# Kernel optimization log

Hardware: AMD Instinct MI355X
Metric: run time of the kernel (lower is better)

## Reference

```python
import jax, jax.numpy as jnp
import numpy as np

HEADS = 4
HID = 32
IN = 128
OUT = 8
N = 50000
E = 1600000


def setup_inputs() -> dict:
    key = jax.random.key(0)
    ks = jax.random.split(key, 12)
    x = jax.random.normal(ks[0], (N, IN), dtype=jnp.float32)
    edge_index = jax.random.randint(ks[1], (2, E), 0, N, dtype=jnp.int64)
    s = 0.05
    W1 = jax.random.normal(ks[2], (IN, HEADS * HID), dtype=jnp.float32) * s
    att_src1 = jax.random.normal(ks[3], (HEADS, HID), dtype=jnp.float32) * s
    att_dst1 = jax.random.normal(ks[4], (HEADS, HID), dtype=jnp.float32) * s
    b1 = jnp.zeros((HEADS * HID,), dtype=jnp.float32)
    W2 = jax.random.normal(ks[5], (HEADS * HID, HEADS * HID), dtype=jnp.float32) * s
    att_src2 = jax.random.normal(ks[6], (HEADS, HID), dtype=jnp.float32) * s
    att_dst2 = jax.random.normal(ks[7], (HEADS, HID), dtype=jnp.float32) * s
    b2 = jnp.zeros((HEADS * HID,), dtype=jnp.float32)
    Wout = jax.random.normal(ks[8], (HEADS * HID, OUT), dtype=jnp.float32) * s
    bout = jnp.zeros((OUT,), dtype=jnp.float32)
    return {"x": x, "edge_index": edge_index, "W1": W1, "att_src1": att_src1,
            "att_dst1": att_dst1, "b1": b1, "W2": W2, "att_src2": att_src2,
            "att_dst2": att_dst2, "b2": b2, "Wout": Wout, "bout": bout}


def gat_conv(x, src, dst, W, att_src, att_dst, b):
    n = x.shape[0]
    h = (x @ W).reshape(n, HEADS, HID)              # [N,H,C]
    a_s = (h * att_src).sum(-1)                      # [N,H]
    a_d = (h * att_dst).sum(-1)                      # [N,H]
    e = jax.nn.leaky_relu(a_s[src] + a_d[dst], 0.2)  # [E,H]
    # scatter-softmax over incoming edges of each destination node
    m = jax.ops.segment_max(e, dst, num_segments=n)
    e = jnp.exp(e - m[dst])
    denom = jax.ops.segment_sum(e, dst, num_segments=n)
    alpha = e / (denom[dst] + 1e-16)                 # [E,H]
    msg = h[src] * alpha[:, :, None]                 # [E,H,C]
    out = jax.ops.segment_sum(msg, dst, num_segments=n)
    return out.reshape(n, HEADS * HID) + b


def reference(x, edge_index, W1, att_src1, att_dst1, b1, W2, att_src2, att_dst2, b2, Wout, bout):
    n = x.shape[0]
    # GATConv adds self-loops by default
    loops = jnp.arange(n, dtype=edge_index.dtype)
    src = jnp.concatenate([edge_index[0], loops])
    dst = jnp.concatenate([edge_index[1], loops])
    # dropout p=0.6 is identity in eval mode
    h = gat_conv(x, src, dst, W1, att_src1, att_dst1, b1)
    h = jax.nn.elu(h)
    h = gat_conv(h, src, dst, W2, att_src2, att_dst2, b2)
    return h @ Wout + bout
```

## Files before the change

kernel.cpp:

```cpp
#include <hip/hip_runtime.h>
#include <hip/hip_fp16.h>
#include <math.h>

#define N_NODES 50000
#define E_EDGES 1600000
#define NE_TOT  (E_EDGES + N_NODES)

#define BSH 7
#define NBKT ((N_NODES + 127) >> 7)
#define EPW 4096
#define NWA ((NE_TOT + EPW - 1) / EPW)

#define CH 128


__device__ __forceinline__ void gemm_att_body(
    int bid, int t, float* Wl, float* xs,
    const float* __restrict__ X, const float* __restrict__ W,
    const float* __restrict__ attS, const float* __restrict__ attD,
    __half* __restrict__ H16, float* __restrict__ a_s, float* __restrict__ a_d) {
    int g = t >> 5, cl = t & 31, c4 = cl * 4;
    int rowbase = bid * 32;
    float4 acc[4];
    #pragma unroll
    for (int rr = 0; rr < 4; rr++) acc[rr] = make_float4(0.f, 0.f, 0.f, 0.f);

    for (int kp = 0; kp < 2; kp++) {
        __syncthreads();
        #pragma unroll
        for (int j = 0; j < 8; j++) {
            int f4 = t + 256 * j;
            int kk = f4 >> 5, cg = f4 & 31;
            *(float4*)&Wl[kk * 128 + cg * 4] =
                *(const float4*)&W[(kp * 64 + kk) * 128 + cg * 4];
        }
        #pragma unroll
        for (int j = 0; j < 2; j++) {
            int f4 = t + 256 * j;
            int r = f4 >> 4, k4 = f4 & 15;
            int grow = rowbase + r;
            float4 xv = make_float4(0.f, 0.f, 0.f, 0.f);
            if (grow < N_NODES) xv = *(const float4*)&X[grow * 128 + kp * 64 + k4 * 4];
            *(float4*)&xs[r * 64 + k4 * 4] = xv;
        }
        __syncthreads();
        #pragma unroll
        for (int k4 = 0; k4 < 16; k4++) {
            float4 xv[4];
            #pragma unroll
            for (int rr = 0; rr < 4; rr++)
                xv[rr] = *(float4*)&xs[(g * 4 + rr) * 64 + k4 * 4];
            #pragma unroll
            for (int kk = 0; kk < 4; kk++) {
                float4 wv = *(float4*)&Wl[(k4 * 4 + kk) * 128 + c4];
                #pragma unroll
                for (int rr = 0; rr < 4; rr++) {
                    float xc = (kk == 0) ? xv[rr].x : (kk == 1) ? xv[rr].y
                             : (kk == 2) ? xv[rr].z : xv[rr].w;
                    acc[rr].x += xc * wv.x;
                    acc[rr].y += xc * wv.y;
                    acc[rr].z += xc * wv.z;
                    acc[rr].w += xc * wv.w;
                }
            }
        }
    }

    float4 as4 = *(const float4*)&attS[c4];
    float4 ad4 = *(const float4*)&attD[c4];
    int head = cl >> 3;
    #pragma unroll
    for (int rr = 0; rr < 4; rr++) {
        int grow = rowbase + g * 4 + rr;
        float4 a = acc[rr];
        if (grow < N_NODES) {
            __half2 lo = __floats2half2_rn(a.x, a.y);
            __half2 hi = __floats2half2_rn(a.z, a.w);
            uint2 pk;
            pk.x = *(unsigned int*)&lo;
            pk.y = *(unsigned int*)&hi;
            *(uint2*)&H16[(size_t)grow * 128 + c4] = pk;
        }
        float ps = a.x * as4.x + a.y * as4.y + a.z * as4.z + a.w * as4.w;
        float pd = a.x * ad4.x + a.y * ad4.y + a.z * ad4.z + a.w * ad4.w;
        ps += __shfl_xor(ps, 1); ps += __shfl_xor(ps, 2); ps += __shfl_xor(ps, 4);
        pd += __shfl_xor(pd, 1); pd += __shfl_xor(pd, 2); pd += __shfl_xor(pd, 4);
        if ((cl & 7) == 0 && grow < N_NODES) {
            a_s[grow * 4 + head] = ps;
            a_d[grow * 4 + head] = pd;
        }
    }
}

__global__ __launch_bounds__(256) void k_hist_gemm(
    const int* __restrict__ ei, int* __restrict__ histG,
    const float* __restrict__ X, const float* __restrict__ W,
    const float* __restrict__ attS, const float* __restrict__ attD,
    __half* __restrict__ H16, float* __restrict__ a_s, float* __restrict__ a_d) {
    __shared__ __align__(16) char smem[40960];
    int t = threadIdx.x;
    if (blockIdx.x < NWA) {
        int* h = (int*)smem;
        for (int i = t; i < NBKT; i += 256) h[i] = 0;
        __syncthreads();
        int base = blockIdx.x * EPW;
        #pragma unroll 4
        for (int j = 0; j < EPW / 256; j++) {
            int e = base + t + 256 * j;
            if (e < NE_TOT) {
                int d = (e < E_EDGES) ? ei[E_EDGES + e] : (e - E_EDGES);
                atomicAdd(&h[d >> BSH], 1);
            }
        }
        __syncthreads();
        for (int i = t; i < NBKT; i += 256) histG[blockIdx.x * NBKT + i] = h[i];
    } else {
        float* Wl = (float*)smem;
        float* xs = (float*)(smem + 32768);
        gemm_att_body(blockIdx.x - NWA, t, Wl, xs, X, W, attS, attD, H16, a_s, a_d);
    }
}

__global__ __launch_bounds__(256) void k_gemm_att(
    const float* __restrict__ X, const float* __restrict__ W,
    const float* __restrict__ attS, const float* __restrict__ attD,
    __half* __restrict__ H16, float* __restrict__ a_s, float* __restrict__ a_d) {
    __shared__ float Wl[64 * 128];
    __shared__ float xs[32 * 64];
    gemm_att_body(blockIdx.x, threadIdx.x, Wl, xs, X, W, attS, attD, H16, a_s, a_d);
}


__global__ __launch_bounds__(512) void k_bktscan(int* __restrict__ histG,
                                                 int* __restrict__ bktTotal) {
    __shared__ int sh[512];
    int b = blockIdx.x;
    int t = threadIdx.x;
    int v = (t < NWA) ? histG[t * NBKT + b] : 0;
    sh[t] = v;
    __syncthreads();
    for (int d = 1; d < 512; d <<= 1) {
        int x = (t >= d) ? sh[t - d] : 0;
        __syncthreads();
        sh[t] += x;
        __syncthreads();
    }
    if (t < NWA) histG[t * NBKT + b] = sh[t] - v;
    if (t == 511) bktTotal[b] = sh[511];
}

__global__ __launch_bounds__(512) void k_bktbase(const int* __restrict__ bktTotal,
                                                 int* __restrict__ bktBase,
                                                 int* __restrict__ row_start) {
    __shared__ int sc[512];
    int t = threadIdx.x;
    int v = (t < NBKT) ? bktTotal[t] : 0;
    sc[t] = v;
    __syncthreads();
    for (int d = 1; d < 512; d <<= 1) {
        int x = (t >= d) ? sc[t - d] : 0;
        __syncthreads();
        sc[t] += x;
        __syncthreads();
    }
    if (t < NBKT) bktBase[t] = sc[t] - v;
    if (t == NBKT - 1) { bktBase[NBKT] = sc[t]; row_start[N_NODES] = sc[t]; }
}

__global__ __launch_bounds__(256) void k_binscatter(const int* __restrict__ ei,
                                                    const int* __restrict__ histG,
                                                    const int* __restrict__ bktBase,
                                                    int2* __restrict__ pairs) {
    __shared__ int lofs[NBKT];
    int t = threadIdx.x;
    for (int i = t; i < NBKT; i += 256)
        lofs[i] = bktBase[i] + histG[blockIdx.x * NBKT + i];
    __syncthreads();
    int base = blockIdx.x * EPW;
    #pragma unroll 4
    for (int j = 0; j < EPW / 256; j++) {
        int e = base + t + 256 * j;
        if (e < NE_TOT) {
            int s, d;
            if (e < E_EDGES) { s = ei[e]; d = ei[E_EDGES + e]; }
            else             { s = d = e - E_EDGES; }
            int pos = atomicAdd(&lofs[d >> BSH], 1);
            pairs[pos] = make_int2(s, d);
        }
    }
}

__global__ __launch_bounds__(256) void k_bucketsort(const int2* __restrict__ pairs,
                                                    const int* __restrict__ bktBase,
                                                    int* __restrict__ row_start,
                                                    int* __restrict__ col) {
    __shared__ int cnt[1 << BSH];
    __shared__ int sc[1 << BSH];
    __shared__ int cur[1 << BSH];
    int b = blockIdx.x, t = threadIdx.x;
    int nbeg = b << BSH;
    int ebeg = bktBase[b], eend = bktBase[b + 1];
    if (t < (1 << BSH)) cnt[t] = 0;
    __syncthreads();
    for (int j = ebeg + t; j < eend; j += 256)
        atomicAdd(&cnt[pairs[j].y - nbeg], 1);
    __syncthreads();
    int v = (t < (1 << BSH)) ? cnt[t] : 0;
    if (t < (1 << BSH)) sc[t] = v;
    __syncthreads();
    for (int d = 1; d < (1 << BSH); d <<= 1) {
        int x = 0;
        if (t < (1 << BSH) && t >= d) x = sc[t - d];
        __syncthreads();
        if (t < (1 << BSH)) sc[t] += x;
        __syncthreads();
    }
    if (t < (1 << BSH)) {
        int pos = ebeg + sc[t] - v;
        cur[t] = pos;
        int node = nbeg + t;
        if (node < N_NODES) row_start[node] = pos;
    }
    __syncthreads();
    for (int j = ebeg + t; j < eend; j += 256) {
        int2 p = pairs[j];
        int pos = atomicAdd(&cur[p.y - nbeg], 1);
        col[pos] = p.x;
    }
}


__device__ inline float sel4(float4 v, int i) {
    float r = v.x;
    if (i == 1) r = v.y;
    if (i == 2) r = v.z;
    if (i == 3) r = v.w;
    return r;
}

__device__ inline float4 expleaky4(float4 a, float4 b) {
    float4 e, p;
    e.x = a.x + b.x; e.x = e.x > 0.f ? e.x : 0.2f * e.x; p.x = __expf(e.x);
    e.y = a.y + b.y; e.y = e.y > 0.f ? e.y : 0.2f * e.y; p.y = __expf(e.y);
    e.z = a.z + b.z; e.z = e.z > 0.f ? e.z : 0.2f * e.z; p.z = __expf(e.z);
    e.w = a.w + b.w; e.w = e.w > 0.f ? e.w : 0.2f * e.w; p.w = __expf(e.w);
    return p;
}

#define ACC8(q, raw)                                              \
    do {                                                          \
        const __half2* hp_ = (const __half2*)&(raw);              \
        float2 f0_ = __half22float2(hp_[0]);                      \
        float2 f1_ = __half22float2(hp_[1]);                      \
        float2 f2_ = __half22float2(hp_[2]);                      \
        float2 f3_ = __half22float2(hp_[3]);                      \
        acc8[0] = fmaf((q), f0_.x, acc8[0]);                      \
        acc8[1] = fmaf((q), f0_.y, acc8[1]);                      \
        acc8[2] = fmaf((q), f1_.x, acc8[2]);                      \
        acc8[3] = fmaf((q), f1_.y, acc8[3]);                      \
        acc8[4] = fmaf((q), f2_.x, acc8[4]);                      \
        acc8[5] = fmaf((q), f2_.y, acc8[5]);                      \
        acc8[6] = fmaf((q), f3_.x, acc8[6]);                      \
        acc8[7] = fmaf((q), f3_.y, acc8[7]);                      \
    } while (0)

template<int MODE>
__global__ __launch_bounds__(256) void k_agg(
    const __half* __restrict__ H16, const float* __restrict__ a_s,
    const float* __restrict__ a_d, const int* __restrict__ row_start,
    const int* __restrict__ col, const float* __restrict__ bias,
    float* __restrict__ Hout,
    const float* __restrict__ Wout, const float* __restrict__ bout,
    float* __restrict__ out) {
    __shared__ float4 eS[4][CH];
    __shared__ int    sS[4][CH];
    __shared__ float  WoT[(MODE == 0) ? 1024 : 1];
    __shared__ float  boL[(MODE == 0) ? 8 : 1];

    if (MODE == 0) {
        for (int j = threadIdx.x; j < 1024; j += 256) {
            int o = j >> 7, k = j & 127;
            WoT[o * 128 + k] = Wout[k * 8 + o];
        }
        if (threadIdx.x < 8) boL[threadIdx.x] = bout[threadIdx.x];
        __syncthreads();
    }

    int wid = threadIdx.x >> 6;
    int lane = threadIdx.x & 63;
    int node = blockIdx.x * 4 + wid;
    if (node >= N_NODES) return;
    int beg = row_start[node], end = row_start[node + 1];
    int deg = end - beg;
    float4 ad4 = *(const float4*)&a_d[node * 4];
    float4* eA = eS[wid];
    int*    srcA = sS[wid];

    float4 s = make_float4(0.f, 0.f, 0.f, 0.f);
    for (int j = beg + lane; j < end; j += 64) {
        int src = col[j];
        float4 av = *(const float4*)&a_s[src * 4];
        float4 p = expleaky4(av, ad4);
        int idx = j - beg;
        if (idx < CH) { srcA[idx] = src; eA[idx] = p; }
        s.x += p.x; s.y += p.y; s.z += p.z; s.w += p.w;
    }
    #pragma unroll
    for (int off = 32; off > 0; off >>= 1) {
        s.x += __shfl_xor(s.x, off);
        s.y += __shfl_xor(s.y, off);
        s.z += __shfl_xor(s.z, off);
        s.w += __shfl_xor(s.w, off);
    }
    float4 inv;
    inv.x = 1.f / (s.x + 1e-16f);
    inv.y = 1.f / (s.y + 1e-16f);
    inv.z = 1.f / (s.z + 1e-16f);
    inv.w = 1.f / (s.w + 1e-16f);

    int eslot = lane >> 4, cl16 = lane & 15, head = cl16 >> 2;
    const __half* hbase = H16 + cl16 * 8;
    const float* pA = (const float*)eA;
    float acc8[8];
    #pragma unroll
    for (int k = 0; k < 8; k++) acc8[k] = 0.f;

    int nst = min(deg, CH);
    int i = eslot;
    for (; i + 12 < nst; i += 16) {
        int s0 = srcA[i];
        int s1 = srcA[i + 4];
        int s2 = srcA[i + 8];
        int s3 = srcA[i + 12];
        float q0 = pA[i * 4 + head];
        float q1 = pA[(i + 4) * 4 + head];
        float q2 = pA[(i + 8) * 4 + head];
        float q3 = pA[(i + 12) * 4 + head];
        float4 r0 = *(const float4*)(hbase + (size_t)s0 * 128);
        float4 r1 = *(const float4*)(hbase + (size_t)s1 * 128);
        float4 r2 = *(const float4*)(hbase + (size_t)s2 * 128);
        float4 r3 = *(const float4*)(hbase + (size_t)s3 * 128);
        ACC8(q0, r0);
        ACC8(q1, r1);
        ACC8(q2, r2);
        ACC8(q3, r3);
    }
    for (; i < nst; i += 4) {
        int src = srcA[i];
        float p = pA[i * 4 + head];
        float4 raw = *(const float4*)(hbase + (size_t)src * 128);
        ACC8(p, raw);
    }
    for (int cb = beg + CH; cb < end; cb += CH) {
        int cnt = min(end - cb, CH);
        for (int idx = lane; idx < cnt; idx += 64) {
            int src = col[cb + idx];
            float4 av = *(const float4*)&a_s[src * 4];
            float4 p = expleaky4(av, ad4);
            srcA[idx] = src; eA[idx] = p;
        }
        for (int ii = eslot; ii < cnt; ii += 4) {
            int src = srcA[ii];
            float p = pA[ii * 4 + head];
            float4 raw = *(const float4*)(hbase + (size_t)src * 128);
            ACC8(p, raw);
        }
    }

    #pragma unroll
    for (int k = 0; k < 8; k++) {
        acc8[k] += __shfl_xor(acc8[k], 16);
        acc8[k] += __shfl_xor(acc8[k], 32);
    }

    float ih = sel4(inv, head);
    if (MODE == 1) {
        if (eslot == 0) {
            const float* bp = &bias[cl16 * 8];
            float o[8];
            #pragma unroll
            for (int k = 0; k < 8; k++) {
                o[k] = acc8[k] * ih + bp[k];
                o[k] = o[k] > 0.f ? o[k] : expm1f(o[k]);
            }
            float* op = &Hout[(size_t)node * 128 + cl16 * 8];
            *(float4*)&op[0] = make_float4(o[0], o[1], o[2], o[3]);
            *(float4*)&op[4] = make_float4(o[4], o[5], o[6], o[7]);
        }
    } else {
        const float* bp = &bias[cl16 * 8];
        float4 oa, ob;
        oa.x = acc8[0] * ih + bp[0]; oa.y = acc8[1] * ih + bp[1];
        oa.z = acc8[2] * ih + bp[2]; oa.w = acc8[3] * ih + bp[3];
        ob.x = acc8[4] * ih + bp[4]; ob.y = acc8[5] * ih + bp[5];
        ob.z = acc8[6] * ih + bp[6]; ob.w = acc8[7] * ih + bp[7];
        int o0 = eslot * 2;
        float p0 = 0.f, p1 = 0.f;
        {
            float4 wa = *(float4*)&WoT[o0 * 128 + cl16 * 8];
            float4 wb = *(float4*)&WoT[o0 * 128 + cl16 * 8 + 4];
            p0 = oa.x * wa.x + oa.y * wa.y + oa.z * wa.z + oa.w * wa.w
               + ob.x * wb.x + ob.y * wb.y + ob.z * wb.z + ob.w * wb.w;
            float4 wc = *(float4*)&WoT[(o0 + 1) * 128 + cl16 * 8];
            float4 wd = *(float4*)&WoT[(o0 + 1) * 128 + cl16 * 8 + 4];
            p1 = oa.x * wc.x + oa.y * wc.y + oa.z * wc.z + oa.w * wc.w
               + ob.x * wd.x + ob.y * wd.y + ob.z * wd.z + ob.w * wd.w;
        }
        #pragma unroll
        for (int d = 1; d <= 8; d <<= 1) {
            p0 += __shfl_xor(p0, d);
            p1 += __shfl_xor(p1, d);
        }
        if (cl16 == 0) {
            float2 ov = make_float2(p0 + boL[o0], p1 + boL[o0 + 1]);
            *(float2*)&out[(size_t)node * 8 + o0] = ov;
        }
    }
}


extern "C" void kernel_launch(void* const* d_in, const int* in_sizes, int n_in,
                              void* d_out, int out_size, void* d_ws, size_t ws_size,
                              hipStream_t stream) {
    const float* x     = (const float*)d_in[0];
    const int*   ei    = (const int*)d_in[1];
    const float* W1    = (const float*)d_in[2];
    const float* attS1 = (const float*)d_in[3];
    const float* attD1 = (const float*)d_in[4];
    const float* b1    = (const float*)d_in[5];
    const float* W2    = (const float*)d_in[6];
    const float* attS2 = (const float*)d_in[7];
    const float* attD2 = (const float*)d_in[8];
    const float* b2    = (const float*)d_in[9];
    const float* Wout  = (const float*)d_in[10];
    const float* bout  = (const float*)d_in[11];
    float* out = (float*)d_out;

    char* ws = (char*)d_ws;
    size_t off = 0;
    auto alloc = [&](size_t bytes) -> void* {
        void* p = ws + off;
        off += (bytes + 255) & ~(size_t)255;
        return p;
    };
    float*  hB        = (float*)alloc((size_t)N_NODES * 128 * 4);
    __half* h16       = (__half*)alloc((size_t)N_NODES * 128 * 2);
    float*  a_s       = (float*)alloc((size_t)N_NODES * 4 * 4);
    float*  a_d       = (float*)alloc((size_t)N_NODES * 4 * 4);
    int*    row_start = (int*)alloc((size_t)(N_NODES + 1) * 4);
    int*    col       = (int*)alloc((size_t)NE_TOT * 4);
    int*    histG     = (int*)alloc((size_t)NWA * NBKT * 4);
    int*    bktTotal  = (int*)alloc((size_t)NBKT * 4);
    int*    bktBase   = (int*)alloc((size_t)(NBKT + 1) * 4);
    int2*   pairs     = (int2*)hB;

    int nbG = (N_NODES + 31) / 32;
    int nbA = (N_NODES + 3) / 4;

    k_hist_gemm<<<NWA + nbG, 256, 0, stream>>>(ei, histG, x, W1, attS1, attD1,
                                               h16, a_s, a_d);
    k_bktscan<<<NBKT, 512, 0, stream>>>(histG, bktTotal);
    k_bktbase<<<1, 512, 0, stream>>>(bktTotal, bktBase, row_start);
    k_binscatter<<<NWA, 256, 0, stream>>>(ei, histG, bktBase, pairs);
    k_bucketsort<<<NBKT, 256, 0, stream>>>(pairs, bktBase, row_start, col);

    k_agg<1><<<nbA, 256, 0, stream>>>(h16, a_s, a_d, row_start, col, b1, hB,
                                      Wout, bout, out);
    k_gemm_att<<<nbG, 256, 0, stream>>>(hB, W2, attS2, attD2, h16, a_s, a_d);
    k_agg<0><<<nbA, 256, 0, stream>>>(h16, a_s, a_d, row_start, col, b2, hB,
                                      Wout, bout, out);
}
```

Measured before the change: 257.2 us.

## Pack edge indices to 16-bit, shrink agg blocks, deepen gather unroll

Edge (dst, src) pairs are packed into one 32-bit word and the CSR column array is stored as 16-bit indices. This halves the bytes moved in the binscatter, bucketsort and both aggregation passes. The aggregation kernel drops to 128-thread blocks and keeps Wout and bout in per-thread registers, so the shared-memory staging and barrier go away. The gather loop also gains an 8-way unrolled stage for more memory-level parallelism. The 16-bit packing only works because the node count is below 65536, and the wider unroll raises register pressure.

```diff
diff --git a/kernel.cpp b/kernel.cpp
--- a/kernel.cpp
+++ b/kernel.cpp
@@ -170,7 +170,7 @@
 __global__ __launch_bounds__(256) void k_binscatter(const int* __restrict__ ei,
                                                     const int* __restrict__ histG,
                                                     const int* __restrict__ bktBase,
-                                                    int2* __restrict__ pairs) {
+                                                    unsigned int* __restrict__ pairs) {
     __shared__ int lofs[NBKT];
     int t = threadIdx.x;
     for (int i = t; i < NBKT; i += 256)
@@ -185,15 +185,15 @@
             if (e < E_EDGES) { s = ei[e]; d = ei[E_EDGES + e]; }
             else             { s = d = e - E_EDGES; }
             int pos = atomicAdd(&lofs[d >> BSH], 1);
-            pairs[pos] = make_int2(s, d);
-        }
-    }
-}
-
-__global__ __launch_bounds__(256) void k_bucketsort(const int2* __restrict__ pairs,
+            pairs[pos] = ((unsigned int)d << 16) | (unsigned int)s;
+        }
+    }
+}
+
+__global__ __launch_bounds__(256) void k_bucketsort(const unsigned int* __restrict__ pairs,
                                                     const int* __restrict__ bktBase,
                                                     int* __restrict__ row_start,
-                                                    int* __restrict__ col) {
+                                                    unsigned short* __restrict__ col) {
     __shared__ int cnt[1 << BSH];
     __shared__ int sc[1 << BSH];
     __shared__ int cur[1 << BSH];
@@ -203,7 +203,7 @@
     if (t < (1 << BSH)) cnt[t] = 0;
     __syncthreads();
     for (int j = ebeg + t; j < eend; j += 256)
-        atomicAdd(&cnt[pairs[j].y - nbeg], 1);
+        atomicAdd(&cnt[(int)(pairs[j] >> 16) - nbeg], 1);
     __syncthreads();
     int v = (t < (1 << BSH)) ? cnt[t] : 0;
     if (t < (1 << BSH)) sc[t] = v;
@@ -223,9 +223,9 @@
     }
     __syncthreads();
     for (int j = ebeg + t; j < eend; j += 256) {
-        int2 p = pairs[j];
-        int pos = atomicAdd(&cur[p.y - nbeg], 1);
-        col[pos] = p.x;
+        unsigned int p = pairs[j];
+        int pos = atomicAdd(&cur[(int)(p >> 16) - nbeg], 1);
+        col[pos] = (unsigned short)(p & 0xFFFFu);
     }
 }
 
@@ -265,31 +265,34 @@
     } while (0)
 
 template<int MODE>
-__global__ __launch_bounds__(256) void k_agg(
+__global__ __launch_bounds__(128) void k_agg(
     const __half* __restrict__ H16, const float* __restrict__ a_s,
     const float* __restrict__ a_d, const int* __restrict__ row_start,
-    const int* __restrict__ col, const float* __restrict__ bias,
+    const unsigned short* __restrict__ col, const float* __restrict__ bias,
     float* __restrict__ Hout,
     const float* __restrict__ Wout, const float* __restrict__ bout,
     float* __restrict__ out) {
-    __shared__ float4 eS[4][CH];
-    __shared__ int    sS[4][CH];
-    __shared__ float  WoT[(MODE == 0) ? 1024 : 1];
-    __shared__ float  boL[(MODE == 0) ? 8 : 1];
-
-    if (MODE == 0) {
-        for (int j = threadIdx.x; j < 1024; j += 256) {
-            int o = j >> 7, k = j & 127;
-            WoT[o * 128 + k] = Wout[k * 8 + o];
-        }
-        if (threadIdx.x < 8) boL[threadIdx.x] = bout[threadIdx.x];
-        __syncthreads();
-    }
+    __shared__ float4 eS[2][CH];
+    __shared__ int    sS[2][CH];
 
     int wid = threadIdx.x >> 6;
     int lane = threadIdx.x & 63;
-    int node = blockIdx.x * 4 + wid;
+    int node = blockIdx.x * 2 + wid;
     if (node >= N_NODES) return;
+
+    int eslot = lane >> 4, cl16 = lane & 15, head = cl16 >> 2;
+
+    float wA[8], wB[8], bo0 = 0.f, bo1 = 0.f;
+    if (MODE == 0) {
+        int o0 = eslot * 2;
+        #pragma unroll
+        for (int k = 0; k < 8; k++) {
+            wA[k] = Wout[(cl16 * 8 + k) * 8 + o0];
+            wB[k] = Wout[(cl16 * 8 + k) * 8 + o0 + 1];
+        }
+        bo0 = bout[o0]; bo1 = bout[o0 + 1];
+    }
+
     int beg = row_start[node], end = row_start[node + 1];
     int deg = end - beg;
     float4 ad4 = *(const float4*)&a_d[node * 4];
@@ -298,7 +301,7 @@
 
     float4 s = make_float4(0.f, 0.f, 0.f, 0.f);
     for (int j = beg + lane; j < end; j += 64) {
-        int src = col[j];
+        int src = (int)col[j];
         float4 av = *(const float4*)&a_s[src * 4];
         float4 p = expleaky4(av, ad4);
         int idx = j - beg;
@@ -318,7 +321,6 @@
     inv.z = 1.f / (s.z + 1e-16f);
     inv.w = 1.f / (s.w + 1e-16f);
 
-    int eslot = lane >> 4, cl16 = lane & 15, head = cl16 >> 2;
     const __half* hbase = H16 + cl16 * 8;
     const float* pA = (const float*)eA;
     float acc8[8];
@@ -327,6 +329,18 @@
 
     int nst = min(deg, CH);
     int i = eslot;
+    for (; i + 28 < nst; i += 32) {
+        int sidx[8]; float qv[8]; float4 rv[8];
+        #pragma unroll
+        for (int k = 0; k < 8; k++) sidx[k] = srcA[i + 4 * k];
+        #pragma unroll
+        for (int k = 0; k < 8; k++) qv[k] = pA[(i + 4 * k) * 4 + head];
+        #pragma unroll
+        for (int k = 0; k < 8; k++)
+            rv[k] = *(const float4*)(hbase + (size_t)sidx[k] * 128);
+        #pragma unroll
+        for (int k = 0; k < 8; k++) ACC8(qv[k], rv[k]);
+    }
     for (; i + 12 < nst; i += 16) {
         int s0 = srcA[i];
         int s1 = srcA[i + 4];
@@ -354,7 +368,7 @@
     for (int cb = beg + CH; cb < end; cb += CH) {
         int cnt = min(end - cb, CH);
         for (int idx = lane; idx < cnt; idx += 64) {
-            int src = col[cb + idx];
+            int src = (int)col[cb + idx];
             float4 av = *(const float4*)&a_s[src * 4];
             float4 p = expleaky4(av, ad4);
             srcA[idx] = src; eA[idx] = p;
@@ -389,22 +403,14 @@
         }
     } else {
         const float* bp = &bias[cl16 * 8];
-        float4 oa, ob;
-        oa.x = acc8[0] * ih + bp[0]; oa.y = acc8[1] * ih + bp[1];
-        oa.z = acc8[2] * ih + bp[2]; oa.w = acc8[3] * ih + bp[3];
-        ob.x = acc8[4] * ih + bp[4]; ob.y = acc8[5] * ih + bp[5];
-        ob.z = acc8[6] * ih + bp[6]; ob.w = acc8[7] * ih + bp[7];
-        int o0 = eslot * 2;
+        float h2[8];
+        #pragma unroll
+        for (int k = 0; k < 8; k++) h2[k] = acc8[k] * ih + bp[k];
         float p0 = 0.f, p1 = 0.f;
-        {
-            float4 wa = *(float4*)&WoT[o0 * 128 + cl16 * 8];
-            float4 wb = *(float4*)&WoT[o0 * 128 + cl16 * 8 + 4];
-            p0 = oa.x * wa.x + oa.y * wa.y + oa.z * wa.z + oa.w * wa.w
-               + ob.x * wb.x + ob.y * wb.y + ob.z * wb.z + ob.w * wb.w;
-            float4 wc = *(float4*)&WoT[(o0 + 1) * 128 + cl16 * 8];
-            float4 wd = *(float4*)&WoT[(o0 + 1) * 128 + cl16 * 8 + 4];
-            p1 = oa.x * wc.x + oa.y * wc.y + oa.z * wc.z + oa.w * wc.w
-               + ob.x * wd.x + ob.y * wd.y + ob.z * wd.z + ob.w * wd.w;
+        #pragma unroll
+        for (int k = 0; k < 8; k++) {
+            p0 = fmaf(h2[k], wA[k], p0);
+            p1 = fmaf(h2[k], wB[k], p1);
         }
         #pragma unroll
         for (int d = 1; d <= 8; d <<= 1) {
@@ -412,7 +418,8 @@
             p1 += __shfl_xor(p1, d);
         }
         if (cl16 == 0) {
-            float2 ov = make_float2(p0 + boL[o0], p1 + boL[o0 + 1]);
+            int o0 = eslot * 2;
+            float2 ov = make_float2(p0 + bo0, p1 + bo1);
             *(float2*)&out[(size_t)node * 8 + o0] = ov;
         }
     }
@@ -443,19 +450,19 @@
         off += (bytes + 255) & ~(size_t)255;
         return p;
     };
-    float*  hB        = (float*)alloc((size_t)N_NODES * 128 * 4);
-    __half* h16       = (__half*)alloc((size_t)N_NODES * 128 * 2);
-    float*  a_s       = (float*)alloc((size_t)N_NODES * 4 * 4);
-    float*  a_d       = (float*)alloc((size_t)N_NODES * 4 * 4);
-    int*    row_start = (int*)alloc((size_t)(N_NODES + 1) * 4);
-    int*    col       = (int*)alloc((size_t)NE_TOT * 4);
-    int*    histG     = (int*)alloc((size_t)NWA * NBKT * 4);
-    int*    bktTotal  = (int*)alloc((size_t)NBKT * 4);
-    int*    bktBase   = (int*)alloc((size_t)(NBKT + 1) * 4);
-    int2*   pairs     = (int2*)hB;
+    float*          hB        = (float*)alloc((size_t)N_NODES * 128 * 4);
+    __half*         h16       = (__half*)alloc((size_t)N_NODES * 128 * 2);
+    float*          a_s       = (float*)alloc((size_t)N_NODES * 4 * 4);
+    float*          a_d       = (float*)alloc((size_t)N_NODES * 4 * 4);
+    int*            row_start = (int*)alloc((size_t)(N_NODES + 1) * 4);
+    unsigned short* col       = (unsigned short*)alloc((size_t)NE_TOT * 2);
+    int*            histG     = (int*)alloc((size_t)NWA * NBKT * 4);
+    int*            bktTotal  = (int*)alloc((size_t)NBKT * 4);
+    int*            bktBase   = (int*)alloc((size_t)(NBKT + 1) * 4);
+    unsigned int*   pairs     = (unsigned int*)hB;
 
     int nbG = (N_NODES + 31) / 32;
-    int nbA = (N_NODES + 3) / 4;
+    int nbA = (N_NODES + 1) / 2;
 
     k_hist_gemm<<<NWA + nbG, 256, 0, stream>>>(ei, histG, x, W1, attS1, attD1,
                                                h16, a_s, a_d);
@@ -464,9 +471,9 @@
     k_binscatter<<<NWA, 256, 0, stream>>>(ei, histG, bktBase, pairs);
     k_bucketsort<<<NBKT, 256, 0, stream>>>(pairs, bktBase, row_start, col);
 
-    k_agg<1><<<nbA, 256, 0, stream>>>(h16, a_s, a_d, row_start, col, b1, hB,
+    k_agg<1><<<nbA, 128, 0, stream>>>(h16, a_s, a_d, row_start, col, b1, hB,
                                       Wout, bout, out);
     k_gemm_att<<<nbG, 256, 0, stream>>>(hB, W2, attS2, attD2, h16, a_s, a_d);
-    k_agg<0><<<nbA, 256, 0, stream>>>(h16, a_s, a_d, row_start, col, b2, hB,
+    k_agg<0><<<nbA, 128, 0, stream>>>(h16, a_s, a_d, row_start, col, b2, hB,
                                       Wout, bout, out);
 }
```

Result: slower. 286.9 us (+11.6%).
